# Kernel tuning notes

Hardware: AMD Instinct MI355X
Metric: run time of the kernel (lower is better)

## Reference

```python
import jax, jax.numpy as jnp
import numpy as np

D = 512      # emb_size
H = 8        # attention heads
E = 8        # num experts
HID = 512    # expert MLP hidden (assumed StandardExpert = 2-layer MLP)
NTOK = 8192  # 8*1024 tokens
W_IMP = 0.01


def setup_inputs() -> dict:
    key = jax.random.key(0)
    ks = jax.random.split(key, 16)
    f = lambda i, shape, s=0.02: (jax.random.normal(ks[i], shape, jnp.float32) * s)
    return {
        "x": jax.random.normal(ks[0], (8, 1024, D), jnp.float32),
        "q": jax.random.normal(ks[1], (NTOK, D), jnp.float32),
        "Wq": f(2, (D, D)), "bq": jnp.zeros((D,), jnp.float32),
        "Wk": f(3, (D, D)), "bk": jnp.zeros((D,), jnp.float32),
        "Wv": f(4, (D, D)), "bv": jnp.zeros((D,), jnp.float32),
        "Wo": f(5, (D, D)), "bo": jnp.zeros((D,), jnp.float32),
        "gate_W": f(6, (D, E)), "gate_b": jnp.zeros((E,), jnp.float32),
        "W1": f(7, (E, D, HID)), "b1": jnp.zeros((E, HID), jnp.float32),
        "W2": f(8, (E, HID, D)), "b2": jnp.zeros((E, D), jnp.float32),
        "top": 2,
    }


def _cross_att(xf, q, Wq, bq, Wk, bk, Wv, bv, Wo, bo):
    # seq_len == 1 on both sides after unsqueeze(1) in the torch code
    N, d = xf.shape
    dh = d // H
    Q = (xf @ Wq + bq).reshape(N, H, dh)
    K = (q @ Wk + bk).reshape(N, H, dh)
    V = (q @ Wv + bv).reshape(N, H, dh)
    scores = jnp.sum(Q * K, axis=-1, keepdims=True) / jnp.sqrt(jnp.float32(dh))  # [N,H,1]
    w = jax.nn.softmax(scores, axis=-1)  # trivially ones (single key), kept for fidelity
    att = (w * V).reshape(N, d)
    return att @ Wo + bo


def reference(x, q, Wq, bq, Wk, bk, Wv, bv, Wo, bo, gate_W, gate_b, W1, b1, W2, b2, top):
    x_shape = x.shape
    xf = x.reshape(-1, x_shape[-1])  # [N, D]
    att = _cross_att(xf, q, Wq, bq, Wk, bk, Wv, bv, Wo, bo)
    gate_logits = att @ gate_W + gate_b
    gate_prob = jax.nn.softmax(gate_logits, axis=-1)  # [N, E] (eval mode: no noise)
    top_w, top_i = jax.lax.top_k(gate_prob, top)       # [N, top]
    top_w = jax.nn.softmax(top_w, axis=-1)
    # combine weights per expert: comb[n,e] = sum_k top_w[n,k] * [top_i[n,k]==e]
    comb = jnp.sum(top_w[..., None] * jax.nn.one_hot(top_i, E, dtype=xf.dtype), axis=1)  # [N, E]
    y = jnp.zeros_like(xf)
    for e in range(E):  # fixed small expert loop; dense compute + mask-combine
        h = jax.nn.relu(xf @ W1[e] + b1[e])
        ye = h @ W2[e] + b2[e]
        y = y + comb[:, e:e + 1] * ye
    importance = gate_prob.sum(axis=0)  # [E]
    # torch.std uses ddof=1
    importance_loss = W_IMP * (jnp.std(importance, ddof=1) / jnp.mean(importance)) ** 2
    return y.reshape(x_shape), gate_prob, importance_loss
```

## Files before the change

kernel.cpp:

```cpp
#include <hip/hip_runtime.h>
#include <math.h>
#include <stdint.h>

#define NTOK 8192
#define DIM  512
#define NEXP 8
#define HIDN 512
#define BM 128
#define BN 128
#define BK 32
#define NT  (DIM / BK)
#define MAXRB 72
#define SLOTS (MAXRB*BM)
#define GBLK (NTOK/16)

typedef _Float16 f16;
typedef __attribute__((ext_vector_type(4))) _Float16 f16x4;
typedef __attribute__((ext_vector_type(8))) _Float16 f16x8;
typedef __attribute__((ext_vector_type(4))) float    f32x4;

__device__ __forceinline__ void gl2lds16(const void* g, void* l) {
  __builtin_amdgcn_global_load_lds(
      (const __attribute__((address_space(1))) unsigned int*)(g),
      (__attribute__((address_space(3))) unsigned int*)(l), 16, 0, 0);
}

__global__ __launch_bounds__(256) void k_prep(
    const float* __restrict__ x, f16* __restrict__ xh,
    const float* __restrict__ W1, const float* __restrict__ W2,
    f16* __restrict__ W1t, f16* __restrict__ W2t, float* __restrict__ y) {
  const int bx = blockIdx.x, tid = threadIdx.x;
  if (bx < 4096) {
    int i4 = (bx * 256 + tid) * 4;
    float4 v = *(const float4*)(x + i4);
    f16x4 o; o.x = (_Float16)v.x; o.y = (_Float16)v.y; o.z = (_Float16)v.z; o.w = (_Float16)v.w;
    *(f16x4*)(xh + i4) = o;
  } else if (bx < 8192) {
    __shared__ float t[32][33];
    int idx = bx - 4096;
    int z = idx >> 8, rem = idx & 255;
    int k0 = (rem >> 4) * 32, n0 = (rem & 15) * 32;
    const float* src = (z < 8 ? W1 : W2) + (size_t)(z & 7) * DIM * DIM;
    f16* dst = (z < 8 ? W1t : W2t) + (size_t)(z & 7) * DIM * DIM;
    int tx = tid & 31, ty = tid >> 5;
    for (int r = ty; r < 32; r += 8) t[r][tx] = src[(size_t)(k0 + r) * DIM + n0 + tx];
    __syncthreads();
    for (int r = ty; r < 32; r += 8) dst[(size_t)(n0 + r) * DIM + k0 + tx] = (f16)t[tx][r];
  } else {
    int b = bx - 8192;
    float4 z4 = {0.f, 0.f, 0.f, 0.f};
#pragma unroll
    for (int it = 0; it < 4; it++)
      *(float4*)(y + (size_t)b * 4096 + it * 1024 + tid * 4) = z4;
  }
}

__global__ void k_foldA(const float* __restrict__ Wo, const float* __restrict__ gW,
                        double* __restrict__ G1) {
  int out = blockIdx.x * 4 + (threadIdx.x >> 6);
  int lane = threadIdx.x & 63;
  int d = out >> 3, e = out & 7;
  double acc = 0.0;
#pragma unroll
  for (int j = 0; j < 8; j++) {
    int k = j * 64 + lane;
    acc += (double)Wo[d * DIM + k] * (double)gW[k * NEXP + e];
  }
#pragma unroll
  for (int off = 32; off; off >>= 1) acc += __shfl_xor(acc, off, 64);
  if (lane == 0) G1[out] = acc;
}

__global__ void k_foldB(const float* __restrict__ Wv, const double* __restrict__ G1,
                        float* __restrict__ Wg, const float* __restrict__ bv,
                        const float* __restrict__ bo, const float* __restrict__ gW,
                        const float* __restrict__ gb, double* __restrict__ bg) {
  int lane = threadIdx.x & 63;
  if (blockIdx.x == 1024) {
    int w = threadIdx.x >> 6;
    for (int e = w; e < NEXP; e += 4) {
      double acc = 0.0;
#pragma unroll
      for (int j = 0; j < 8; j++) {
        int d = j * 64 + lane;
        acc += (double)bv[d] * G1[d * NEXP + e] + (double)bo[d] * (double)gW[d * NEXP + e];
      }
#pragma unroll
      for (int off = 32; off; off >>= 1) acc += __shfl_xor(acc, off, 64);
      if (lane == 0) bg[e] = acc + (double)gb[e];
    }
    return;
  }
  int out = blockIdx.x * 4 + (threadIdx.x >> 6);
  int d = out >> 3, e = out & 7;
  double acc = 0.0;
#pragma unroll
  for (int j = 0; j < 8; j++) {
    int k = j * 64 + lane;
    acc += (double)Wv[d * DIM + k] * G1[k * NEXP + e];
  }
#pragma unroll
  for (int off = 32; off; off >>= 1) acc += __shfl_xor(acc, off, 64);
  if (lane == 0) Wg[out] = (float)acc;
}

__global__ __launch_bounds__(256) void k_gate(
    const float* __restrict__ q, const float* __restrict__ Wg,
    const double* __restrict__ bg, float* __restrict__ gp_out,
    int* __restrict__ e1a, int* __restrict__ e2a,
    float* __restrict__ w1a, float* __restrict__ w2a,
    int* __restrict__ r1a, int* __restrict__ r2a, int* __restrict__ hist,
    float* __restrict__ gpsum) {
  __shared__ float qs[16 * 513];
  __shared__ float ps[16][8];
  __shared__ int cnt[16];
  const int tid = threadIdx.x;
  const int tok0 = blockIdx.x * 16;

  for (int i = tid; i < 16 * 512; i += 256) {
    int r = i >> 9, c = i & 511;
    qs[r * 513 + c] = q[(size_t)(tok0 + r) * DIM + c];
  }
  if (tid < 16) cnt[tid] = 0;
  __syncthreads();

  const int e = tid & 7;
  const int half = (tid >> 3) & 1;
  const int tl = tid >> 4;
  const float* qrow = qs + tl * 513 + half * 256;
  const float* wcol = Wg + half * 256 * NEXP + e;

  double a0 = 0, a1 = 0, a2 = 0, a3 = 0;
#pragma unroll 4
  for (int j = 0; j < 256; j += 4) {
    a0 += (double)qrow[j]     * (double)wcol[(size_t)j * NEXP];
    a1 += (double)qrow[j + 1] * (double)wcol[(size_t)(j + 1) * NEXP];
    a2 += (double)qrow[j + 2] * (double)wcol[(size_t)(j + 2) * NEXP];
    a3 += (double)qrow[j + 3] * (double)wcol[(size_t)(j + 3) * NEXP];
  }
  double acc = (a0 + a1) + (a2 + a3);
  acc += __shfl_xor(acc, 8, 64);

  double l = acc + bg[e];
  double m = l;
#pragma unroll
  for (int off = 1; off < 8; off <<= 1) m = fmax(m, __shfl_xor(m, off, 64));
  float ex = expf((float)(l - m));
  float s = ex;
#pragma unroll
  for (int off = 1; off < 8; off <<= 1) s += __shfl_xor(s, off, 64);
  float pf = ex / s;
  int tok = tok0 + tl;
  if (half == 0) { gp_out[(size_t)tok * NEXP + e] = pf; ps[tl][e] = pf; }

  double v1 = l; int i1 = e;
#pragma unroll
  for (int off = 1; off < 8; off <<= 1) {
    double ov = __shfl_xor(v1, off, 64);
    int oi = __shfl_xor(i1, off, 64);
    if (ov > v1 || (ov == v1 && oi < i1)) { v1 = ov; i1 = oi; }
  }
  double v2 = (e == i1) ? -1e300 : l; int i2 = e;
#pragma unroll
  for (int off = 1; off < 8; off <<= 1) {
    double ov = __shfl_xor(v2, off, 64);
    int oi = __shfl_xor(i2, off, 64);
    if (ov > v2 || (ov == v2 && oi < i2)) { v2 = ov; i2 = oi; }
  }
  float p1 = __shfl(pf, (tl << 4) + i1, 64);
  float p2 = __shfl(pf, (tl << 4) + i2, 64);
  if (e == 0 && half == 0) {
    float ev = expf(p2 - p1);
    float iw = 1.0f / (1.0f + ev);
    e1a[tok] = i1; e2a[tok] = i2;
    w1a[tok] = iw; w2a[tok] = ev * iw;
    r1a[tok] = atomicAdd(&cnt[i1], 1);
    r2a[tok] = atomicAdd(&cnt[8 + i2], 1);
  }
  __syncthreads();
  if (tid < 16) hist[blockIdx.x * 16 + tid] = cnt[tid];
  if (tid < 8) {
    float ssum = 0.f;
#pragma unroll
    for (int r = 0; r < 16; r++) ssum += ps[r][tid];
    gpsum[blockIdx.x * 8 + tid] = ssum;
  }
}

__global__ __launch_bounds__(1024) void k_scan2(const int* __restrict__ hist,
                                                int* __restrict__ blockbase,
                                                int* __restrict__ aoff,
                                                int* __restrict__ counts,
                                                int* __restrict__ toks,
                                                const float* __restrict__ gpsum,
                                                float* __restrict__ loss) {
  __shared__ int tot[16];
  __shared__ int s_ao[16];
  __shared__ double imp[8];
  const int c = threadIdx.x >> 6;
  const int l = threadIdx.x & 63;
  int v[GBLK / 64];
  int s = 0;
#pragma unroll
  for (int j = 0; j < GBLK / 64; j++) {
    v[j] = hist[((l * (GBLK / 64) + j) << 4) + c];
    s += v[j];
  }
  int incl = s;
#pragma unroll
  for (int off = 1; off < 64; off <<= 1) {
    int t = __shfl_up(incl, off, 64);
    if (l >= off) incl += t;
  }
  int run = incl - s;
#pragma unroll
  for (int j = 0; j < GBLK / 64; j++) {
    blockbase[((l * (GBLK / 64) + j) << 4) + c] = run;
    run += v[j];
  }
  if (l == 63) tot[c] = incl;
  __syncthreads();
  if (threadIdx.x == 0) {
    int o0 = 0, o1 = 0;
    for (int e = 0; e < NEXP; e++) {
      counts[e] = tot[e];
      aoff[e] = o0; s_ao[e] = o0; o0 += (tot[e] + BM - 1) / BM * BM;
      counts[8 + e] = tot[8 + e];
      aoff[9 + e] = o1; s_ao[8 + e] = o1; o1 += (tot[8 + e] + BM - 1) / BM * BM;
    }
    aoff[8] = o0; aoff[17] = o1;
  }
  __syncthreads();
  const int cnt_c = tot[c];
  const int padded = (cnt_c + BM - 1) / BM * BM;
  const int base = ((c >> 3) ? SLOTS : 0) + s_ao[c];
  for (int sidx = cnt_c + l; sidx < padded; sidx += 64)
    toks[base + sidx] = 0;
  if (c < 8) {
    double a = 0.0;
#pragma unroll
    for (int j = 0; j < GBLK / 64; j++)
      a += (double)gpsum[(size_t)(l + j * 64) * 8 + c];
#pragma unroll
    for (int off = 32; off; off >>= 1) a += __shfl_xor(a, off, 64);
    if (l == 0) imp[c] = a;
  }
  __syncthreads();
  if (threadIdx.x == 0) {
    double mn = 0.0;
    for (int e = 0; e < 8; e++) mn += imp[e];
    mn *= (1.0 / 8.0);
    double var = 0.0;
    for (int e = 0; e < 8; e++) { double d = imp[e] - mn; var += d * d; }
    var *= (1.0 / 7.0);
    double r = sqrt(var) / mn;
    loss[0] = (float)(0.01 * r * r);
  }
}

__global__ void k_scatter2(const int* __restrict__ e1a, const int* __restrict__ e2a,
                           const float* __restrict__ w1a, const float* __restrict__ w2a,
                           const int* __restrict__ r1a, const int* __restrict__ r2a,
                           const int* __restrict__ blockbase, const int* __restrict__ aoff,
                           int* __restrict__ toks, float* __restrict__ wsl) {
  int n = blockIdx.x * 256 + threadIdx.x;
  int blk = n >> 4;
  int e1 = e1a[n];
  int slot = aoff[e1] + blockbase[(blk << 4) + e1] + r1a[n];
  toks[slot] = n; wsl[slot] = w1a[n];
  int e2 = e2a[n];
  slot = SLOTS + aoff[9 + e2] + blockbase[(blk << 4) + 8 + e2] + r2a[n];
  toks[slot] = n; wsl[slot] = w2a[n];
}

template <int MODE>
__global__ __launch_bounds__(256) void k_expert(
    const f16* __restrict__ Asrc, const f16* __restrict__ Wt,
    const float* __restrict__ bias, const int* __restrict__ toks,
    const float* __restrict__ wsl, const int* __restrict__ aoff,
    const int* __restrict__ counts, f16* __restrict__ Hout,
    float* __restrict__ y) {
  const int klist = blockIdx.z;
  const int* ao = aoff + klist * 9;
  const int slot0 = blockIdx.x * BM;
  if (slot0 >= ao[8]) return;
  int e = 0;
#pragma unroll
  for (int t = 1; t <= 7; t++) if (slot0 >= ao[t]) e = t;

  const int n0 = blockIdx.y * BN;
  const int tid = threadIdx.x, lane = tid & 63, wid = tid >> 6;

  __shared__ __align__(16) f16 As[2][BM * BK];
  __shared__ __align__(16) f16 Bs[2][BN * BK];

  const int srow = wid * 16 + (lane >> 2);
  const int scol = (lane & 3) * 8;
  const f16* arow[2];
  const f16* brow[2];
  int loff[2];
#pragma unroll
  for (int rnd = 0; rnd < 2; rnd++) {
    int r = srow + rnd * 64;
    if (MODE == 0) {
      int tk = toks[klist * SLOTS + slot0 + r];
      arow[rnd] = Asrc + (size_t)tk * DIM + scol;
    } else {
      arow[rnd] = Asrc + (size_t)(klist * SLOTS + slot0 + r) * HIDN + scol;
    }
    brow[rnd] = Wt + ((size_t)e * DIM + n0 + r) * DIM + scol;
    loff[rnd] = (wid * 16 + rnd * 64) * BK;
  }

  f32x4 acc[4][4] = {};
  const int wr = wid >> 1, wc = wid & 1;
  const int fr = lane & 15, kb = (lane >> 4) * 8;

#define STAGE(buf, ks)                                  \
  {                                                     \
    _Pragma("unroll")                                   \
    for (int rnd = 0; rnd < 2; rnd++) {                 \
      gl2lds16(arow[rnd] + (ks), As[buf] + loff[rnd]);  \
      gl2lds16(brow[rnd] + (ks), Bs[buf] + loff[rnd]);  \
    }                                                   \
  }

  STAGE(0, 0);
#pragma unroll
  for (int t = 0; t < NT; t++) {
    const int cur = t & 1;
    if (t + 1 < NT) {
      STAGE(cur ^ 1, (t + 1) * BK);
      asm volatile("s_waitcnt vmcnt(4)" ::: "memory");
    } else {
      asm volatile("s_waitcnt vmcnt(0)" ::: "memory");
    }
    __builtin_amdgcn_s_barrier();
    f16x8 af[4], bf[4];
#pragma unroll
    for (int m = 0; m < 4; m++)
      af[m] = *(const f16x8*)(As[cur] + (wr * 64 + m * 16 + fr) * BK + kb);
#pragma unroll
    for (int n = 0; n < 4; n++)
      bf[n] = *(const f16x8*)(Bs[cur] + (wc * 64 + n * 16 + fr) * BK + kb);
#pragma unroll
    for (int m = 0; m < 4; m++)
#pragma unroll
      for (int n = 0; n < 4; n++)
        acc[m][n] = __builtin_amdgcn_mfma_f32_16x16x32_f16(af[m], bf[n], acc[m][n], 0, 0, 0);
    __builtin_amdgcn_s_barrier();
  }
#undef STAGE

  float bcol[4];
#pragma unroll
  for (int n = 0; n < 4; n++)
    bcol[n] = bias[e * ((MODE == 0) ? HIDN : DIM) + n0 + wc * 64 + n * 16 + fr];

  if (MODE == 0) {
#pragma unroll
    for (int m = 0; m < 4; m++)
#pragma unroll
      for (int r4 = 0; r4 < 4; r4++) {
        int slot = slot0 + wr * 64 + m * 16 + (lane >> 4) * 4 + r4;
#pragma unroll
        for (int n = 0; n < 4; n++) {
          int col = n0 + wc * 64 + n * 16 + fr;
          float v = acc[m][n][r4] + bcol[n];
          Hout[(size_t)(klist * SLOTS + slot) * HIDN + col] = (f16)fmaxf(v, 0.f);
        }
      }
  } else {
    const int vend = ao[e] + counts[klist * 8 + e];
#pragma unroll
    for (int m = 0; m < 4; m++)
#pragma unroll
      for (int r4 = 0; r4 < 4; r4++) {
        int slot = slot0 + wr * 64 + m * 16 + (lane >> 4) * 4 + r4;
        if (slot < vend) {
          int tk = toks[klist * SLOTS + slot];
          float w = wsl[klist * SLOTS + slot];
#pragma unroll
          for (int n = 0; n < 4; n++) {
            int col = n0 + wc * 64 + n * 16 + fr;
            float v = (acc[m][n][r4] + bcol[n]) * w;
            __hip_atomic_fetch_add(&y[(size_t)tk * DIM + col], v,
                                   __ATOMIC_RELAXED, __HIP_MEMORY_SCOPE_AGENT);
          }
        }
      }
  }
}

extern "C" void kernel_launch(void* const* d_in, const int* in_sizes, int n_in,
                              void* d_out, int out_size, void* d_ws, size_t ws_size,
                              hipStream_t stream) {
  const float* x  = (const float*)d_in[0];
  const float* q  = (const float*)d_in[1];
  const float* Wv = (const float*)d_in[6];
  const float* bv = (const float*)d_in[7];
  const float* Wo = (const float*)d_in[8];
  const float* bo = (const float*)d_in[9];
  const float* gW = (const float*)d_in[10];
  const float* gb = (const float*)d_in[11];
  const float* W1 = (const float*)d_in[12];
  const float* b1 = (const float*)d_in[13];
  const float* W2 = (const float*)d_in[14];
  const float* b2 = (const float*)d_in[15];

  float* out = (float*)d_out;
  float* y_out = out;
  float* gp_out = out + (size_t)NTOK * DIM;
  float* loss_out = gp_out + (size_t)NTOK * NEXP;

  uint8_t* w = (uint8_t*)d_ws;
  size_t o = 0;
  auto alloc = [&](size_t bytes) -> void* {
    void* p = w + o;
    o = (o + bytes + 255) & ~(size_t)255;
    return p;
  };
  f16* xh      = (f16*)alloc((size_t)NTOK * DIM * 2);
  f16* W1t     = (f16*)alloc((size_t)NEXP * DIM * HIDN * 2);
  f16* W2t     = (f16*)alloc((size_t)NEXP * DIM * HIDN * 2);
  f16* Hbuf    = (f16*)alloc((size_t)2 * SLOTS * HIDN * 2);
  double* G1   = (double*)alloc((size_t)DIM * NEXP * 8);
  float* Wg    = (float*)alloc((size_t)DIM * NEXP * 4);
  double* bg   = (double*)alloc(NEXP * 8);
  int* e1a     = (int*)alloc(NTOK * 4);
  int* e2a     = (int*)alloc(NTOK * 4);
  float* w1a   = (float*)alloc(NTOK * 4);
  float* w2a   = (float*)alloc(NTOK * 4);
  int* r1a     = (int*)alloc(NTOK * 4);
  int* r2a     = (int*)alloc(NTOK * 4);
  int* hist    = (int*)alloc((size_t)GBLK * 16 * 4);
  int* bbase   = (int*)alloc((size_t)GBLK * 16 * 4);
  float* gpsum = (float*)alloc((size_t)GBLK * 8 * 4);
  int* counts  = (int*)alloc(16 * 4);
  int* aoff    = (int*)alloc(18 * 4);
  int* toks    = (int*)alloc((size_t)2 * SLOTS * 4);
  float* wsl   = (float*)alloc((size_t)2 * SLOTS * 4);
  (void)ws_size; (void)in_sizes; (void)n_in; (void)out_size;

  k_prep<<<9216, 256, 0, stream>>>(x, xh, W1, W2, W1t, W2t, y_out);
  k_foldA<<<1024, 256, 0, stream>>>(Wo, gW, G1);
  k_foldB<<<1025, 256, 0, stream>>>(Wv, G1, Wg, bv, bo, gW, gb, bg);
  k_gate<<<GBLK, 256, 0, stream>>>(q, Wg, bg, gp_out, e1a, e2a, w1a, w2a, r1a, r2a, hist, gpsum);
  k_scan2<<<1, 1024, 0, stream>>>(hist, bbase, aoff, counts, toks, gpsum, loss_out);
  k_scatter2<<<NTOK / 256, 256, 0, stream>>>(e1a, e2a, w1a, w2a, r1a, r2a, bbase, aoff, toks, wsl);
  k_expert<0><<<dim3(MAXRB, 4, 2), 256, 0, stream>>>(xh, W1t, b1, toks, wsl, aoff, counts,
                                                     Hbuf, nullptr);
  k_expert<1><<<dim3(MAXRB, 4, 2), 256, 0, stream>>>(Hbuf, W2t, b2, toks, wsl, aoff, counts,
                                                     nullptr, y_out);
}
```

Before: 114.3 us.

## Replace atomic expert combine with two ordered store/accumulate passes and single-buffer LDS

```diff
diff --git a/kernel.cpp b/kernel.cpp
--- a/kernel.cpp
+++ b/kernel.cpp
@@ -9,7 +9,6 @@
 #define BM 128
 #define BN 128
 #define BK 32
-#define NT  (DIM / BK)
 #define MAXRB 72
 #define SLOTS (MAXRB*BM)
 #define GBLK (NTOK/16)
@@ -28,14 +27,14 @@
 __global__ __launch_bounds__(256) void k_prep(
     const float* __restrict__ x, f16* __restrict__ xh,
     const float* __restrict__ W1, const float* __restrict__ W2,
-    f16* __restrict__ W1t, f16* __restrict__ W2t, float* __restrict__ y) {
+    f16* __restrict__ W1t, f16* __restrict__ W2t) {
   const int bx = blockIdx.x, tid = threadIdx.x;
   if (bx < 4096) {
     int i4 = (bx * 256 + tid) * 4;
     float4 v = *(const float4*)(x + i4);
     f16x4 o; o.x = (_Float16)v.x; o.y = (_Float16)v.y; o.z = (_Float16)v.z; o.w = (_Float16)v.w;
     *(f16x4*)(xh + i4) = o;
-  } else if (bx < 8192) {
+  } else {
     __shared__ float t[32][33];
     int idx = bx - 4096;
     int z = idx >> 8, rem = idx & 255;
@@ -46,12 +45,6 @@
     for (int r = ty; r < 32; r += 8) t[r][tx] = src[(size_t)(k0 + r) * DIM + n0 + tx];
     __syncthreads();
     for (int r = ty; r < 32; r += 8) dst[(size_t)(n0 + r) * DIM + k0 + tx] = (f16)t[tx][r];
-  } else {
-    int b = bx - 8192;
-    float4 z4 = {0.f, 0.f, 0.f, 0.f};
-#pragma unroll
-    for (int it = 0; it < 4; it++)
-      *(float4*)(y + (size_t)b * 4096 + it * 1024 + tid * 4) = z4;
   }
 }
 
@@ -280,7 +273,7 @@
     const float* __restrict__ wsl, const int* __restrict__ aoff,
     const int* __restrict__ counts, f16* __restrict__ Hout,
     float* __restrict__ y) {
-  const int klist = blockIdx.z;
+  const int klist = (MODE == 0) ? blockIdx.z : (MODE == 2 ? 1 : 0);
   const int* ao = aoff + klist * 9;
   const int slot0 = blockIdx.x * BM;
   if (slot0 >= ao[8]) return;
@@ -291,14 +284,15 @@
   const int n0 = blockIdx.y * BN;
   const int tid = threadIdx.x, lane = tid & 63, wid = tid >> 6;
 
-  __shared__ __align__(16) f16 As[2][BM * BK];
-  __shared__ __align__(16) f16 Bs[2][BN * BK];
+  __shared__ __align__(16) f16 As[BM * BK];
+  __shared__ __align__(16) f16 Bs[BN * BK];
 
   const int srow = wid * 16 + (lane >> 2);
   const int scol = (lane & 3) * 8;
   const f16* arow[2];
   const f16* brow[2];
-  int loff[2];
+  f16* alds[2];
+  f16* blds[2];
 #pragma unroll
   for (int rnd = 0; rnd < 2; rnd++) {
     int r = srow + rnd * 64;
@@ -309,48 +303,35 @@
       arow[rnd] = Asrc + (size_t)(klist * SLOTS + slot0 + r) * HIDN + scol;
     }
     brow[rnd] = Wt + ((size_t)e * DIM + n0 + r) * DIM + scol;
-    loff[rnd] = (wid * 16 + rnd * 64) * BK;
+    alds[rnd] = As + (wid * 16 + rnd * 64) * BK;
+    blds[rnd] = Bs + (wid * 16 + rnd * 64) * BK;
   }
 
   f32x4 acc[4][4] = {};
   const int wr = wid >> 1, wc = wid & 1;
   const int fr = lane & 15, kb = (lane >> 4) * 8;
 
-#define STAGE(buf, ks)                                  \
-  {                                                     \
-    _Pragma("unroll")                                   \
-    for (int rnd = 0; rnd < 2; rnd++) {                 \
-      gl2lds16(arow[rnd] + (ks), As[buf] + loff[rnd]);  \
-      gl2lds16(brow[rnd] + (ks), Bs[buf] + loff[rnd]);  \
-    }                                                   \
-  }
-
-  STAGE(0, 0);
-#pragma unroll
-  for (int t = 0; t < NT; t++) {
-    const int cur = t & 1;
-    if (t + 1 < NT) {
-      STAGE(cur ^ 1, (t + 1) * BK);
-      asm volatile("s_waitcnt vmcnt(4)" ::: "memory");
-    } else {
-      asm volatile("s_waitcnt vmcnt(0)" ::: "memory");
+  for (int ks = 0; ks < DIM; ks += BK) {
+    __syncthreads();
+#pragma unroll
+    for (int rnd = 0; rnd < 2; rnd++) {
+      gl2lds16(arow[rnd] + ks, alds[rnd]);
+      gl2lds16(brow[rnd] + ks, blds[rnd]);
     }
-    __builtin_amdgcn_s_barrier();
+    __syncthreads();
     f16x8 af[4], bf[4];
 #pragma unroll
     for (int m = 0; m < 4; m++)
-      af[m] = *(const f16x8*)(As[cur] + (wr * 64 + m * 16 + fr) * BK + kb);
+      af[m] = *(const f16x8*)(As + (wr * 64 + m * 16 + fr) * BK + kb);
 #pragma unroll
     for (int n = 0; n < 4; n++)
-      bf[n] = *(const f16x8*)(Bs[cur] + (wc * 64 + n * 16 + fr) * BK + kb);
+      bf[n] = *(const f16x8*)(Bs + (wc * 64 + n * 16 + fr) * BK + kb);
 #pragma unroll
     for (int m = 0; m < 4; m++)
 #pragma unroll
       for (int n = 0; n < 4; n++)
         acc[m][n] = __builtin_amdgcn_mfma_f32_16x16x32_f16(af[m], bf[n], acc[m][n], 0, 0, 0);
-    __builtin_amdgcn_s_barrier();
-  }
-#undef STAGE
+  }
 
   float bcol[4];
 #pragma unroll
@@ -384,8 +365,9 @@
           for (int n = 0; n < 4; n++) {
             int col = n0 + wc * 64 + n * 16 + fr;
             float v = (acc[m][n][r4] + bcol[n]) * w;
-            __hip_atomic_fetch_add(&y[(size_t)tk * DIM + col], v,
-                                   __ATOMIC_RELAXED, __HIP_MEMORY_SCOPE_AGENT);
+            size_t oi = (size_t)tk * DIM + col;
+            if (MODE == 1) y[oi] = v;
+            else y[oi] += v;
           }
         }
       }
@@ -442,7 +424,7 @@
   float* wsl   = (float*)alloc((size_t)2 * SLOTS * 4);
   (void)ws_size; (void)in_sizes; (void)n_in; (void)out_size;
 
-  k_prep<<<9216, 256, 0, stream>>>(x, xh, W1, W2, W1t, W2t, y_out);
+  k_prep<<<8192, 256, 0, stream>>>(x, xh, W1, W2, W1t, W2t);
   k_foldA<<<1024, 256, 0, stream>>>(Wo, gW, G1);
   k_foldB<<<1025, 256, 0, stream>>>(Wv, G1, Wg, bv, bo, gW, gb, bg);
   k_gate<<<GBLK, 256, 0, stream>>>(q, Wg, bg, gp_out, e1a, e2a, w1a, w2a, r1a, r2a, hist, gpsum);
@@ -450,6 +432,8 @@
   k_scatter2<<<NTOK / 256, 256, 0, stream>>>(e1a, e2a, w1a, w2a, r1a, r2a, bbase, aoff, toks, wsl);
   k_expert<0><<<dim3(MAXRB, 4, 2), 256, 0, stream>>>(xh, W1t, b1, toks, wsl, aoff, counts,
                                                      Hbuf, nullptr);
-  k_expert<1><<<dim3(MAXRB, 4, 2), 256, 0, stream>>>(Hbuf, W2t, b2, toks, wsl, aoff, counts,
+  k_expert<1><<<dim3(MAXRB, 4, 1), 256, 0, stream>>>(Hbuf, W2t, b2, toks, wsl, aoff, counts,
                                                      nullptr, y_out);
-}
+  k_expert<2><<<dim3(MAXRB, 4, 1), 256, 0, stream>>>(Hbuf, W2t, b2, toks, wsl, aoff, counts,
+                                                     nullptr, y_out);
+}
```

New measurement: 116.7 us. +2.1%, slower.

## Replace atomic output accumulation with store-then-add passes and merge foldA into prep

Applied to the files above, without the earlier changes.

```diff
diff --git a/kernel.cpp b/kernel.cpp
--- a/kernel.cpp
+++ b/kernel.cpp
@@ -28,7 +28,9 @@
 __global__ __launch_bounds__(256) void k_prep(
     const float* __restrict__ x, f16* __restrict__ xh,
     const float* __restrict__ W1, const float* __restrict__ W2,
-    f16* __restrict__ W1t, f16* __restrict__ W2t, float* __restrict__ y) {
+    f16* __restrict__ W1t, f16* __restrict__ W2t,
+    const float* __restrict__ Wo, const float* __restrict__ gW,
+    double* __restrict__ G1) {
   const int bx = blockIdx.x, tid = threadIdx.x;
   if (bx < 4096) {
     int i4 = (bx * 256 + tid) * 4;
@@ -47,28 +49,19 @@
     __syncthreads();
     for (int r = ty; r < 32; r += 8) dst[(size_t)(n0 + r) * DIM + k0 + tx] = (f16)t[tx][r];
   } else {
-    int b = bx - 8192;
-    float4 z4 = {0.f, 0.f, 0.f, 0.f};
-#pragma unroll
-    for (int it = 0; it < 4; it++)
-      *(float4*)(y + (size_t)b * 4096 + it * 1024 + tid * 4) = z4;
-  }
-}
-
-__global__ void k_foldA(const float* __restrict__ Wo, const float* __restrict__ gW,
-                        double* __restrict__ G1) {
-  int out = blockIdx.x * 4 + (threadIdx.x >> 6);
-  int lane = threadIdx.x & 63;
-  int d = out >> 3, e = out & 7;
-  double acc = 0.0;
-#pragma unroll
-  for (int j = 0; j < 8; j++) {
-    int k = j * 64 + lane;
-    acc += (double)Wo[d * DIM + k] * (double)gW[k * NEXP + e];
-  }
-#pragma unroll
-  for (int off = 32; off; off >>= 1) acc += __shfl_xor(acc, off, 64);
-  if (lane == 0) G1[out] = acc;
+    int out = (bx - 8192) * 4 + (tid >> 6);
+    int lane = tid & 63;
+    int d = out >> 3, e = out & 7;
+    double acc = 0.0;
+#pragma unroll
+    for (int j = 0; j < 8; j++) {
+      int k = j * 64 + lane;
+      acc += (double)Wo[d * DIM + k] * (double)gW[k * NEXP + e];
+    }
+#pragma unroll
+    for (int off = 32; off; off >>= 1) acc += __shfl_xor(acc, off, 64);
+    if (lane == 0) G1[out] = acc;
+  }
 }
 
 __global__ void k_foldB(const float* __restrict__ Wv, const double* __restrict__ G1,
@@ -280,7 +273,7 @@
     const float* __restrict__ wsl, const int* __restrict__ aoff,
     const int* __restrict__ counts, f16* __restrict__ Hout,
     float* __restrict__ y) {
-  const int klist = blockIdx.z;
+  const int klist = (MODE == 0) ? blockIdx.z : (MODE == 2 ? 1 : 0);
   const int* ao = aoff + klist * 9;
   const int slot0 = blockIdx.x * BM;
   if (slot0 >= ao[8]) return;
@@ -326,7 +319,7 @@
   }
 
   STAGE(0, 0);
-#pragma unroll
+#pragma unroll 2
   for (int t = 0; t < NT; t++) {
     const int cur = t & 1;
     if (t + 1 < NT) {
@@ -335,7 +328,11 @@
     } else {
       asm volatile("s_waitcnt vmcnt(0)" ::: "memory");
     }
+    __builtin_amdgcn_sched_barrier(0);
     __builtin_amdgcn_s_barrier();
+    asm volatile("" ::: "memory");
+    __builtin_amdgcn_sched_barrier(0);
+
     f16x8 af[4], bf[4];
 #pragma unroll
     for (int m = 0; m < 4; m++)
@@ -348,7 +345,12 @@
 #pragma unroll
       for (int n = 0; n < 4; n++)
         acc[m][n] = __builtin_amdgcn_mfma_f32_16x16x32_f16(af[m], bf[n], acc[m][n], 0, 0, 0);
+
+    asm volatile("s_waitcnt lgkmcnt(0)" ::: "memory");
+    __builtin_amdgcn_sched_barrier(0);
     __builtin_amdgcn_s_barrier();
+    asm volatile("" ::: "memory");
+    __builtin_amdgcn_sched_barrier(0);
   }
 #undef STAGE
 
@@ -384,8 +386,9 @@
           for (int n = 0; n < 4; n++) {
             int col = n0 + wc * 64 + n * 16 + fr;
             float v = (acc[m][n][r4] + bcol[n]) * w;
-            __hip_atomic_fetch_add(&y[(size_t)tk * DIM + col], v,
-                                   __ATOMIC_RELAXED, __HIP_MEMORY_SCOPE_AGENT);
+            size_t oi = (size_t)tk * DIM + col;
+            if (MODE == 1) y[oi] = v;
+            else y[oi] += v;
           }
         }
       }
@@ -442,14 +445,15 @@
   float* wsl   = (float*)alloc((size_t)2 * SLOTS * 4);
   (void)ws_size; (void)in_sizes; (void)n_in; (void)out_size;
 
-  k_prep<<<9216, 256, 0, stream>>>(x, xh, W1, W2, W1t, W2t, y_out);
-  k_foldA<<<1024, 256, 0, stream>>>(Wo, gW, G1);
+  k_prep<<<9216, 256, 0, stream>>>(x, xh, W1, W2, W1t, W2t, Wo, gW, G1);
   k_foldB<<<1025, 256, 0, stream>>>(Wv, G1, Wg, bv, bo, gW, gb, bg);
   k_gate<<<GBLK, 256, 0, stream>>>(q, Wg, bg, gp_out, e1a, e2a, w1a, w2a, r1a, r2a, hist, gpsum);
   k_scan2<<<1, 1024, 0, stream>>>(hist, bbase, aoff, counts, toks, gpsum, loss_out);
   k_scatter2<<<NTOK / 256, 256, 0, stream>>>(e1a, e2a, w1a, w2a, r1a, r2a, bbase, aoff, toks, wsl);
   k_expert<0><<<dim3(MAXRB, 4, 2), 256, 0, stream>>>(xh, W1t, b1, toks, wsl, aoff, counts,
                                                      Hbuf, nullptr);
-  k_expert<1><<<dim3(MAXRB, 4, 2), 256, 0, stream>>>(Hbuf, W2t, b2, toks, wsl, aoff, counts,
+  k_expert<1><<<dim3(MAXRB, 4, 1), 256, 0, stream>>>(Hbuf, W2t, b2, toks, wsl, aoff, counts,
                                                      nullptr, y_out);
-}
+  k_expert<2><<<dim3(MAXRB, 4, 1), 256, 0, stream>>>(Hbuf, W2t, b2, toks, wsl, aoff, counts,
+                                                     nullptr, y_out);
+}
```

New measurement: 119.4 us. 1.04x slower.
